# Optimization experiments

Hardware: AMD Instinct MI355X
Metric: run time of the kernel (lower is better)

Reference implementation:

```python
import jax, jax.numpy as jnp
import numpy as np

BITS = 4
SIGNED_MIN, SIGNED_MAX = -(2 ** (BITS - 1)), 2 ** (BITS - 1) - 1      # int4: [-8, 7]
UNSIGNED_MIN, UNSIGNED_MAX = 0, 2 ** BITS - 1                          # uint4: [0, 15]
INT32_MIN, INT32_MAX = -(2.0 ** 31), 2.0 ** 31 - 1


def fake_quant(x, scale, qmin, qmax):
    """Brevitas-style fake quantization with straight-through rounding."""
    q = jnp.clip(jnp.round(x / scale), qmin, qmax) * scale
    # STE: identity gradient through round/clip
    return x + jax.lax.stop_gradient(q - x)


def weight_scale(W):
    # Brevitas default weight quantizer: per-tensor scale from max-abs stats
    return jax.lax.stop_gradient(jnp.max(jnp.abs(W))) / SIGNED_MAX


def setup_inputs() -> dict:
    key = jax.random.key(0)
    ks = jax.random.split(key, 5)
    B, S, D, F = 4, 2048, 2048, 8192
    return {
        "x": jax.random.normal(ks[0], (B, S, D), dtype=jnp.float32),
        "W1": jax.random.normal(ks[1], (F, D), dtype=jnp.float32) * 0.02,
        "b1": jax.random.normal(ks[2], (F,), dtype=jnp.float32) * 0.02,
        "W2": jax.random.normal(ks[3], (D, F), dtype=jnp.float32) * 0.02,
        "b2": jax.random.normal(ks[4], (D,), dtype=jnp.float32) * 0.02,
        "s_act1": jnp.full((1,), 0.1, dtype=jnp.float32),
        "s_act2": jnp.full((1,), 0.1, dtype=jnp.float32),
    }


def reference(x, W1, b1, W2, b2, s_act1, s_act2):
    s1 = s_act1[0]
    s2 = s_act2[0]

    # quantizer_1: signed int4 QuantIdentity on input
    x_q = fake_quant(x, s1, SIGNED_MIN, SIGNED_MAX)

    # w_1: int4 weight QuantLinear with Int32Bias (bias scale = in_scale * w_scale)
    sw1 = weight_scale(W1)
    W1_q = fake_quant(W1, sw1, SIGNED_MIN, SIGNED_MAX)
    b1_q = fake_quant(b1, s1 * sw1, INT32_MIN, INT32_MAX)
    h = jnp.einsum("bsd,fd->bsf", x_q, W1_q) + b1_q  # [B, S, d_ff]

    # quantizer_2: QuantReLU -> unsigned int4 fake-quant of relu(h)
    h_q = fake_quant(jax.nn.relu(h), s2, UNSIGNED_MIN, UNSIGNED_MAX)
    # dropout: identity in eval mode

    # w_2: int4 weight QuantLinear, input scale = s2
    sw2 = weight_scale(W2)
    W2_q = fake_quant(W2, sw2, SIGNED_MIN, SIGNED_MAX)
    b2_q = fake_quant(b2, s2 * sw2, INT32_MIN, INT32_MAX)
    out = jnp.einsum("bsf,df->bsd", h_q, W2_q) + b2_q  # [B, S, d_model]
    return out
```

## Files before the change

kernel.cpp:

```cpp
#include <hip/hip_runtime.h>

typedef int int32x4 __attribute__((ext_vector_type(4)));
typedef int int32x16 __attribute__((ext_vector_type(16)));

__global__ void maxabs_kernel(const float* __restrict__ x, int n4,
                              unsigned* __restrict__ out) {
    float m = 0.f;
    int i = blockIdx.x * blockDim.x + threadIdx.x;
    int stride = gridDim.x * blockDim.x;
    const float4* x4 = (const float4*)x;
    for (int j = i; j < n4; j += stride) {
        float4 v = x4[j];
        m = fmaxf(m, fmaxf(fmaxf(fabsf(v.x), fabsf(v.y)),
                           fmaxf(fabsf(v.z), fabsf(v.w))));
    }
#pragma unroll
    for (int off = 32; off; off >>= 1)
        m = fmaxf(m, __shfl_down(m, off, 64));
    __shared__ float wm[4];
    int ln = threadIdx.x & 63, wv = threadIdx.x >> 6;
    if (ln == 0) wm[wv] = m;
    __syncthreads();
    if (threadIdx.x == 0) {
        float bm = fmaxf(fmaxf(wm[0], wm[1]), fmaxf(wm[2], wm[3]));
        atomicMax(out, __float_as_uint(bm));
    }
}

__global__ void quant_kernel(const float* __restrict__ x, int n4,
                             const float* __restrict__ sptr, float sdiv,
                             float lo, float hi, char* __restrict__ out) {
    float s = sptr[0] / sdiv;
    int i = blockIdx.x * blockDim.x + threadIdx.x;
    int stride = gridDim.x * blockDim.x;
    const float4* x4 = (const float4*)x;
    int* o4 = (int*)out;
    for (int j = i; j < n4; j += stride) {
        float4 v = x4[j];
        int a = (int)fminf(fmaxf(rintf(v.x / s), lo), hi);
        int b = (int)fminf(fmaxf(rintf(v.y / s), lo), hi);
        int c = (int)fminf(fmaxf(rintf(v.z / s), lo), hi);
        int d = (int)fminf(fmaxf(rintf(v.w / s), lo), hi);
        o4[j] = (a & 255) | ((b & 255) << 8) | ((c & 255) << 16) | ((d & 255) << 24);
    }
}

template <bool FIRST>
__global__ __launch_bounds__(256, 2)
void gemm_i8_kernel(const char* __restrict__ A, const char* __restrict__ B,
                    int M, int N, int K,
                    const float* __restrict__ sa_ptr,
                    const float* __restrict__ wmax_ptr,
                    const float* __restrict__ bias,
                    const float* __restrict__ s2_ptr,
                    char* __restrict__ out8, float* __restrict__ outf) {
    __shared__ __align__(16) char lA[128 * 128];
    __shared__ __align__(16) char lB[128 * 128];

    const int tid = threadIdx.x;
    const int wv = tid >> 6, ln = tid & 63;
    const int l31 = ln & 31, hi5 = ln >> 5;
    const int wr = wv >> 1, wc = wv & 1;

    const int gx = gridDim.x;
    const int nwg = gx * gridDim.y;
    const int orig = blockIdx.y * gx + blockIdx.x;
    const int q = nwg >> 3, r8 = nwg & 7;
    const int xcd = orig & 7, idx = orig >> 3;
    const int wg = (xcd < r8 ? xcd * (q + 1) : r8 * (q + 1) + (xcd - r8) * q) + idx;
    const long m0 = (long)(wg / gx) * 128;
    const long n0 = (long)(wg % gx) * 128;

    int32x16 acc[2][2] = {};

    const int nkt = K >> 7;
    for (int kt = 0; kt < nkt; ++kt) {
        const long k0 = (long)kt << 7;
#pragma unroll
        for (int r = 0; r < 4; ++r) {
            int s = r * 256 + tid;
            int row = s >> 3;
            int ch = s & 7;
            int sch = ch ^ (row & 7);
            long ga = (m0 + row) * K + k0 + sch * 16;
            long gb = (n0 + row) * K + k0 + sch * 16;
            int lbase = (r * 256 + wv * 64) * 16;
            __builtin_amdgcn_global_load_lds(
                (const __attribute__((address_space(1))) void*)(A + ga),
                (__attribute__((address_space(3))) void*)(lA + lbase), 16, 0, 0);
            __builtin_amdgcn_global_load_lds(
                (const __attribute__((address_space(1))) void*)(B + gb),
                (__attribute__((address_space(3))) void*)(lB + lbase), 16, 0, 0);
        }
        __syncthreads();

        int32x4 af[2][4], bf[2][4];
#pragma unroll
        for (int fm = 0; fm < 2; ++fm)
#pragma unroll
            for (int ks = 0; ks < 4; ++ks) {
                int row = wr * 64 + fm * 32 + l31;
                int ch = ks * 2 + hi5;
                af[fm][ks] = *(const int32x4*)(lA + row * 128 + ((ch ^ (row & 7)) * 16));
            }
#pragma unroll
        for (int fn = 0; fn < 2; ++fn)
#pragma unroll
            for (int ks = 0; ks < 4; ++ks) {
                int col = wc * 64 + fn * 32 + l31;
                int ch = ks * 2 + hi5;
                bf[fn][ks] = *(const int32x4*)(lB + col * 128 + ((ch ^ (col & 7)) * 16));
            }

#pragma unroll
        for (int ks = 0; ks < 4; ++ks)
#pragma unroll
            for (int fm = 0; fm < 2; ++fm)
#pragma unroll
                for (int fn = 0; fn < 2; ++fn)
                    acc[fm][fn] = __builtin_amdgcn_mfma_i32_32x32x32_i8(
                        af[fm][ks], bf[fn][ks], acc[fm][fn], 0, 0, 0);
        __syncthreads();
    }

    float sa = sa_ptr[0];
    float sw = wmax_ptr[0] / 7.0f;
    float sab = sa * sw;
    float s2v = FIRST ? s2_ptr[0] : 0.f;

#pragma unroll
    for (int fn = 0; fn < 2; ++fn) {
        long col = n0 + wc * 64 + fn * 32 + l31;
        float bq = rintf(bias[col] / sab) * sab;
#pragma unroll
        for (int fm = 0; fm < 2; ++fm) {
            long rbase = m0 + wr * 64 + fm * 32 + 4 * hi5;
#pragma unroll
            for (int reg = 0; reg < 16; ++reg) {
                long row = rbase + (reg & 3) + 8 * (reg >> 2);
                float h = sab * (float)acc[fm][fn][reg] + bq;
                long off = row * N + col;
                if constexpr (FIRST) {
                    h = fmaxf(h, 0.f);
                    float qv = fminf(fmaxf(rintf(h / s2v), 0.f), 15.f);
                    out8[off] = (char)(int)qv;
                } else {
                    outf[off] = h;
                }
            }
        }
    }
}

extern "C" void kernel_launch(void* const* d_in, const int* in_sizes, int n_in,
                              void* d_out, int out_size, void* d_ws, size_t ws_size,
                              hipStream_t stream) {
    const float* x  = (const float*)d_in[0];
    const float* W1 = (const float*)d_in[1];
    const float* b1 = (const float*)d_in[2];
    const float* W2 = (const float*)d_in[3];
    const float* b2 = (const float*)d_in[4];
    const float* s1 = (const float*)d_in[5];
    const float* s2 = (const float*)d_in[6];

    const int M = 8192, D = 2048, F = 8192;

    char* ws = (char*)d_ws;
    unsigned* mx1 = (unsigned*)ws;
    unsigned* mx2 = (unsigned*)(ws + 4);
    char* xq  = ws + 256;
    char* w1q = xq + (size_t)M * D;
    char* w2q = w1q + (size_t)F * D;
    char* hq  = w2q + (size_t)D * F;

    hipMemsetAsync(d_ws, 0, 8, stream);

    maxabs_kernel<<<2048, 256, 0, stream>>>(W1, (F * D) >> 2, mx1);
    maxabs_kernel<<<2048, 256, 0, stream>>>(W2, (D * F) >> 2, mx2);

    quant_kernel<<<2048, 256, 0, stream>>>(x,  (M * D) >> 2, s1, 1.f, -8.f, 7.f, xq);
    quant_kernel<<<2048, 256, 0, stream>>>(W1, (F * D) >> 2, (const float*)mx1, 7.f, -8.f, 7.f, w1q);
    quant_kernel<<<2048, 256, 0, stream>>>(W2, (D * F) >> 2, (const float*)mx2, 7.f, -8.f, 7.f, w2q);

    gemm_i8_kernel<true><<<dim3(F / 128, M / 128), 256, 0, stream>>>(
        xq, w1q, M, F, D, s1, (const float*)mx1, b1, s2, hq, nullptr);

    gemm_i8_kernel<false><<<dim3(D / 128, M / 128), 256, 0, stream>>>(
        hq, w2q, M, D, F, s2, (const float*)mx2, b2, nullptr, nullptr, (float*)d_out);
}
```

Baseline: 429.6 us.

## Pre-tile quantized operands into LDS-ready blocks and fuse prep kernels

Quantization kernels now write int8 operands in a blocked 128x128 tile layout with 16-byte chunk-major ordering, so each GEMM workgroup streams one contiguous 16KB block per k-step and reads LDS without swizzle. The first GEMM writes its int8 activations directly in that tiled layout for the second GEMM. The prep work is merged from five launches into two, with the max-abs pass and the x quantization sharing one launch. The XCD-aware workgroup remapping is dropped, and the MFMA section is wrapped with s_setprio. Dropping the swizzle may cause LDS bank conflicts on the fragment reads, and losing the remap may reduce L2 locality.

New measurement: 451.8 us. 1.05x slower.

```diff
diff --git a/kernel.cpp b/kernel.cpp
--- a/kernel.cpp
+++ b/kernel.cpp
@@ -3,52 +3,82 @@
 typedef int int32x4 __attribute__((ext_vector_type(4)));
 typedef int int32x16 __attribute__((ext_vector_type(16)));
 
-__global__ void maxabs_kernel(const float* __restrict__ x, int n4,
-                              unsigned* __restrict__ out) {
-    float m = 0.f;
-    int i = blockIdx.x * blockDim.x + threadIdx.x;
+
+__global__ void prep_kernel(const float* __restrict__ W1,
+                            const float* __restrict__ W2,
+                            const float* __restrict__ x, int n4,
+                            int Kx, int kshiftx,
+                            const float* __restrict__ s1,
+                            unsigned* __restrict__ mx, int* __restrict__ xq) {
+    int i0 = blockIdx.x * blockDim.x + threadIdx.x;
     int stride = gridDim.x * blockDim.x;
-    const float4* x4 = (const float4*)x;
-    for (int j = i; j < n4; j += stride) {
-        float4 v = x4[j];
-        m = fmaxf(m, fmaxf(fmaxf(fabsf(v.x), fabsf(v.y)),
-                           fmaxf(fabsf(v.z), fabsf(v.w))));
-    }
-#pragma unroll
-    for (int off = 32; off; off >>= 1)
-        m = fmaxf(m, __shfl_down(m, off, 64));
-    __shared__ float wm[4];
-    int ln = threadIdx.x & 63, wv = threadIdx.x >> 6;
-    if (ln == 0) wm[wv] = m;
-    __syncthreads();
-    if (threadIdx.x == 0) {
-        float bm = fmaxf(fmaxf(wm[0], wm[1]), fmaxf(wm[2], wm[3]));
-        atomicMax(out, __float_as_uint(bm));
-    }
-}
-
-__global__ void quant_kernel(const float* __restrict__ x, int n4,
-                             const float* __restrict__ sptr, float sdiv,
-                             float lo, float hi, char* __restrict__ out) {
-    float s = sptr[0] / sdiv;
-    int i = blockIdx.x * blockDim.x + threadIdx.x;
+    if (blockIdx.y < 2) {
+        const float4* x4 = (const float4*)(blockIdx.y ? W2 : W1);
+        float m = 0.f;
+        for (int j = i0; j < n4; j += stride) {
+            float4 v = x4[j];
+            m = fmaxf(m, fmaxf(fmaxf(fabsf(v.x), fabsf(v.y)),
+                               fmaxf(fabsf(v.z), fabsf(v.w))));
+        }
+#pragma unroll
+        for (int off = 32; off; off >>= 1)
+            m = fmaxf(m, __shfl_down(m, off, 64));
+        __shared__ float wm[4];
+        int ln = threadIdx.x & 63, wv = threadIdx.x >> 6;
+        if (ln == 0) wm[wv] = m;
+        __syncthreads();
+        if (threadIdx.x == 0) {
+            float bm = fmaxf(fmaxf(wm[0], wm[1]), fmaxf(wm[2], wm[3]));
+            atomicMax(mx + blockIdx.y, __float_as_uint(bm));
+        }
+    } else {
+        float s = s1[0];
+        for (int o = i0; o < n4; o += stride) {
+            int blk = o >> 12, i = o & 4095;
+            int ch = i >> 9, row = (i >> 2) & 127, w = i & 3;
+            int rowblk = blk >> kshiftx, kblk = blk & ((1 << kshiftx) - 1);
+            long srcoff = (long)(rowblk * 128 + row) * Kx + (kblk << 7) + (ch << 4) + (w << 2);
+            float4 f = *(const float4*)(x + srcoff);
+            int a = (int)fminf(fmaxf(rintf(f.x / s), -8.f), 7.f);
+            int b = (int)fminf(fmaxf(rintf(f.y / s), -8.f), 7.f);
+            int c = (int)fminf(fmaxf(rintf(f.z / s), -8.f), 7.f);
+            int d = (int)fminf(fmaxf(rintf(f.w / s), -8.f), 7.f);
+            xq[o] = (a & 255) | ((b & 255) << 8) | ((c & 255) << 16) | ((d & 255) << 24);
+        }
+    }
+}
+
+__global__ void quantW_kernel(const float* __restrict__ W1,
+                              const float* __restrict__ W2, int n4,
+                              int K1, int ks1, int K2, int ks2,
+                              const unsigned* __restrict__ mx,
+                              int* __restrict__ w1q, int* __restrict__ w2q) {
+    const int y = blockIdx.y;
+    const float* src = y ? W2 : W1;
+    int* out = y ? w2q : w1q;
+    const int K = y ? K2 : K1;
+    const int kshift = y ? ks2 : ks1;
+    float s = __uint_as_float(mx[y]) / 7.0f;
+    int i0 = blockIdx.x * blockDim.x + threadIdx.x;
     int stride = gridDim.x * blockDim.x;
-    const float4* x4 = (const float4*)x;
-    int* o4 = (int*)out;
-    for (int j = i; j < n4; j += stride) {
-        float4 v = x4[j];
-        int a = (int)fminf(fmaxf(rintf(v.x / s), lo), hi);
-        int b = (int)fminf(fmaxf(rintf(v.y / s), lo), hi);
-        int c = (int)fminf(fmaxf(rintf(v.z / s), lo), hi);
-        int d = (int)fminf(fmaxf(rintf(v.w / s), lo), hi);
-        o4[j] = (a & 255) | ((b & 255) << 8) | ((c & 255) << 16) | ((d & 255) << 24);
+    for (int o = i0; o < n4; o += stride) {
+        int blk = o >> 12, i = o & 4095;
+        int ch = i >> 9, row = (i >> 2) & 127, w = i & 3;
+        int rowblk = blk >> kshift, kblk = blk & ((1 << kshift) - 1);
+        long srcoff = (long)(rowblk * 128 + row) * K + (kblk << 7) + (ch << 4) + (w << 2);
+        float4 f = *(const float4*)(src + srcoff);
+        int a = (int)fminf(fmaxf(rintf(f.x / s), -8.f), 7.f);
+        int b = (int)fminf(fmaxf(rintf(f.y / s), -8.f), 7.f);
+        int c = (int)fminf(fmaxf(rintf(f.z / s), -8.f), 7.f);
+        int d = (int)fminf(fmaxf(rintf(f.w / s), -8.f), 7.f);
+        out[o] = (a & 255) | ((b & 255) << 8) | ((c & 255) << 16) | ((d & 255) << 24);
     }
 }
 
 template <bool FIRST>
 __global__ __launch_bounds__(256, 2)
 void gemm_i8_kernel(const char* __restrict__ A, const char* __restrict__ B,
-                    int M, int N, int K,
+                    int N, int nkt,
                     const float* __restrict__ sa_ptr,
                     const float* __restrict__ wmax_ptr,
                     const float* __restrict__ bias,
@@ -62,36 +92,25 @@
     const int l31 = ln & 31, hi5 = ln >> 5;
     const int wr = wv >> 1, wc = wv & 1;
 
-    const int gx = gridDim.x;
-    const int nwg = gx * gridDim.y;
-    const int orig = blockIdx.y * gx + blockIdx.x;
-    const int q = nwg >> 3, r8 = nwg & 7;
-    const int xcd = orig & 7, idx = orig >> 3;
-    const int wg = (xcd < r8 ? xcd * (q + 1) : r8 * (q + 1) + (xcd - r8) * q) + idx;
-    const long m0 = (long)(wg / gx) * 128;
-    const long n0 = (long)(wg % gx) * 128;
-
     int32x16 acc[2][2] = {};
 
-    const int nkt = K >> 7;
+    const char* pa = A + ((size_t)blockIdx.y * nkt << 14);
+    const char* pb = B + ((size_t)blockIdx.x * nkt << 14);
+
     for (int kt = 0; kt < nkt; ++kt) {
-        const long k0 = (long)kt << 7;
 #pragma unroll
         for (int r = 0; r < 4; ++r) {
-            int s = r * 256 + tid;
-            int row = s >> 3;
-            int ch = s & 7;
-            int sch = ch ^ (row & 7);
-            long ga = (m0 + row) * K + k0 + sch * 16;
-            long gb = (n0 + row) * K + k0 + sch * 16;
+            int off = (r * 256 + tid) * 16;
             int lbase = (r * 256 + wv * 64) * 16;
             __builtin_amdgcn_global_load_lds(
-                (const __attribute__((address_space(1))) void*)(A + ga),
+                (const __attribute__((address_space(1))) void*)(pa + off),
                 (__attribute__((address_space(3))) void*)(lA + lbase), 16, 0, 0);
             __builtin_amdgcn_global_load_lds(
-                (const __attribute__((address_space(1))) void*)(B + gb),
+                (const __attribute__((address_space(1))) void*)(pb + off),
                 (__attribute__((address_space(3))) void*)(lB + lbase), 16, 0, 0);
         }
+        pa += 16384;
+        pb += 16384;
         __syncthreads();
 
         int32x4 af[2][4], bf[2][4];
@@ -101,7 +120,7 @@
             for (int ks = 0; ks < 4; ++ks) {
                 int row = wr * 64 + fm * 32 + l31;
                 int ch = ks * 2 + hi5;
-                af[fm][ks] = *(const int32x4*)(lA + row * 128 + ((ch ^ (row & 7)) * 16));
+                af[fm][ks] = *(const int32x4*)(lA + ch * 2048 + row * 16);
             }
 #pragma unroll
         for (int fn = 0; fn < 2; ++fn)
@@ -109,9 +128,10 @@
             for (int ks = 0; ks < 4; ++ks) {
                 int col = wc * 64 + fn * 32 + l31;
                 int ch = ks * 2 + hi5;
-                bf[fn][ks] = *(const int32x4*)(lB + col * 128 + ((ch ^ (col & 7)) * 16));
+                bf[fn][ks] = *(const int32x4*)(lB + ch * 2048 + col * 16);
             }
 
+        __builtin_amdgcn_s_setprio(1);
 #pragma unroll
         for (int ks = 0; ks < 4; ++ks)
 #pragma unroll
@@ -120,32 +140,36 @@
                 for (int fn = 0; fn < 2; ++fn)
                     acc[fm][fn] = __builtin_amdgcn_mfma_i32_32x32x32_i8(
                         af[fm][ks], bf[fn][ks], acc[fm][fn], 0, 0, 0);
+        __builtin_amdgcn_s_setprio(0);
         __syncthreads();
     }
 
     float sa = sa_ptr[0];
-    float sw = wmax_ptr[0] / 7.0f;
+    float sw = __uint_as_float(((const unsigned*)wmax_ptr)[0]) / 7.0f;
     float sab = sa * sw;
     float s2v = FIRST ? s2_ptr[0] : 0.f;
 
+    char* hblk = FIRST ? out8 + (((size_t)blockIdx.y * gridDim.x + blockIdx.x) << 14)
+                       : nullptr;
+
 #pragma unroll
     for (int fn = 0; fn < 2; ++fn) {
-        long col = n0 + wc * 64 + fn * 32 + l31;
+        int lc = wc * 64 + fn * 32 + l31;
+        long col = (long)blockIdx.x * 128 + lc;
         float bq = rintf(bias[col] / sab) * sab;
 #pragma unroll
         for (int fm = 0; fm < 2; ++fm) {
-            long rbase = m0 + wr * 64 + fm * 32 + 4 * hi5;
+            int lr0 = wr * 64 + fm * 32 + (hi5 << 2);
 #pragma unroll
             for (int reg = 0; reg < 16; ++reg) {
-                long row = rbase + (reg & 3) + 8 * (reg >> 2);
+                int lr = lr0 + (reg & 3) + 8 * (reg >> 2);
                 float h = sab * (float)acc[fm][fn][reg] + bq;
-                long off = row * N + col;
                 if constexpr (FIRST) {
                     h = fmaxf(h, 0.f);
                     float qv = fminf(fmaxf(rintf(h / s2v), 0.f), 15.f);
-                    out8[off] = (char)(int)qv;
+                    hblk[(lc >> 4) * 2048 + lr * 16 + (lc & 15)] = (char)(int)qv;
                 } else {
-                    outf[off] = h;
+                    outf[((long)blockIdx.y * 128 + lr) * N + col] = h;
                 }
             }
         }
@@ -166,8 +190,7 @@
     const int M = 8192, D = 2048, F = 8192;
 
     char* ws = (char*)d_ws;
-    unsigned* mx1 = (unsigned*)ws;
-    unsigned* mx2 = (unsigned*)(ws + 4);
+    unsigned* mx = (unsigned*)ws;
     char* xq  = ws + 256;
     char* w1q = xq + (size_t)M * D;
     char* w2q = w1q + (size_t)F * D;
@@ -175,16 +198,17 @@
 
     hipMemsetAsync(d_ws, 0, 8, stream);
 
-    maxabs_kernel<<<2048, 256, 0, stream>>>(W1, (F * D) >> 2, mx1);
-    maxabs_kernel<<<2048, 256, 0, stream>>>(W2, (D * F) >> 2, mx2);
-
-    quant_kernel<<<2048, 256, 0, stream>>>(x,  (M * D) >> 2, s1, 1.f, -8.f, 7.f, xq);
-    quant_kernel<<<2048, 256, 0, stream>>>(W1, (F * D) >> 2, (const float*)mx1, 7.f, -8.f, 7.f, w1q);
-    quant_kernel<<<2048, 256, 0, stream>>>(W2, (D * F) >> 2, (const float*)mx2, 7.f, -8.f, 7.f, w2q);
+    const int n4 = (F * D) >> 2;
+    prep_kernel<<<dim3(2048, 3), 256, 0, stream>>>(
+        W1, W2, x, n4, D, 4, s1, mx, (int*)xq);
+
+    quantW_kernel<<<dim3(2048, 2), 256, 0, stream>>>(
+        W1, W2, n4, D, 4, F, 6, mx, (int*)w1q, (int*)w2q);
 
     gemm_i8_kernel<true><<<dim3(F / 128, M / 128), 256, 0, stream>>>(
-        xq, w1q, M, F, D, s1, (const float*)mx1, b1, s2, hq, nullptr);
+        xq, w1q, F, D / 128, s1, (const float*)mx, b1, s2, hq, nullptr);
 
     gemm_i8_kernel<false><<<dim3(D / 128, M / 128), 256, 0, stream>>>(
-        hq, w2q, M, D, F, s2, (const float*)mx2, b2, nullptr, nullptr, (float*)d_out);
-}
+        hq, w2q, D, F / 128, s2, (const float*)(mx + 1), b2, nullptr, nullptr,
+        (float*)d_out);
+}
```
